# Performance work log

Hardware: AMD Instinct MI355X
Metric: run time of the kernel (lower is better)

## Reference

```python
import jax, jax.numpy as jnp
import numpy as np

N, E, B = 400000, 800000, 16384
MAX_DEG = 10  # PyG MFConv default max_degree -> 11 weight sets
EPS = 1e-5


def setup_inputs() -> dict:
    key = jax.random.key(0)
    ks = jax.random.split(key, 32)
    d = {}
    d["x"] = jax.random.normal(ks[0], (N, 8), jnp.float32)
    d["edge_index"] = jax.random.randint(ks[1], (2, E), 0, N)
    d["batch"] = jnp.sort(jax.random.randint(ks[2], (N,), 0, B))
    d["x_mord"] = jax.random.normal(ks[3], (B, 862), jnp.float32)
    D = MAX_DEG + 1
    # MFConv degree-dependent weights: Wl (with bias) applied to neighbor sum, Wr (no bias) to self.
    d["Wl1"] = jax.random.normal(ks[4], (D, 32, 8), jnp.float32) * 0.2
    d["bl1"] = jnp.zeros((D, 32), jnp.float32)
    d["Wr1"] = jax.random.normal(ks[5], (D, 32, 8), jnp.float32) * 0.2
    d["Wl2"] = jax.random.normal(ks[6], (D, 32, 32), jnp.float32) * 0.1
    d["bl2"] = jnp.zeros((D, 32), jnp.float32)
    d["Wr2"] = jax.random.normal(ks[7], (D, 32, 32), jnp.float32) * 0.1
    d["Wl3"] = jax.random.normal(ks[8], (D, 32, 32), jnp.float32) * 0.1
    d["bl3"] = jnp.zeros((D, 32), jnp.float32)
    d["Wr3"] = jax.random.normal(ks[9], (D, 32, 32), jnp.float32) * 0.1
    # Dense MLP head
    d["W_fc1"] = jax.random.normal(ks[10], (512, 862), jnp.float32) * 0.03
    d["b_fc1"] = jnp.zeros((512,), jnp.float32)
    d["g1"] = jnp.ones((512,), jnp.float32)
    d["be1"] = jnp.zeros((512,), jnp.float32)
    d["W_fc2"] = jax.random.normal(ks[11], (128, 512), jnp.float32) * 0.04
    d["b_fc2"] = jnp.zeros((128,), jnp.float32)
    d["g2"] = jnp.ones((128,), jnp.float32)
    d["be2"] = jnp.zeros((128,), jnp.float32)
    d["W_fc3"] = jax.random.normal(ks[12], (64, 128), jnp.float32) * 0.09
    d["b_fc3"] = jnp.zeros((64,), jnp.float32)
    d["g3"] = jnp.ones((64,), jnp.float32)
    d["be3"] = jnp.zeros((64,), jnp.float32)
    d["W_out"] = jax.random.normal(ks[13], (1, 96), jnp.float32) * 0.1
    d["b_out"] = jnp.zeros((1,), jnp.float32)
    return d


def _mfconv(x, src, dst, deg_idx, Wl, bl, Wr):
    # h_i = sum_{j in N(i)} x_j  (source_to_target aggregation)
    h = jax.ops.segment_sum(x[src], dst, num_segments=x.shape[0])
    Wl_n = Wl[deg_idx]   # [N, out, in]
    Wr_n = Wr[deg_idx]
    return (jnp.einsum('noi,ni->no', Wl_n, h) + bl[deg_idx]
            + jnp.einsum('noi,ni->no', Wr_n, x))


def _bn_train(h, g, b):
    mu = jnp.mean(h, axis=0)
    var = jnp.mean((h - mu) ** 2, axis=0)  # biased, as torch BN training
    return (h - mu) * jax.lax.rsqrt(var + EPS) * g + b


def reference(x, edge_index, batch, x_mord,
              Wl1, bl1, Wr1, Wl2, bl2, Wr2, Wl3, bl3, Wr3,
              W_fc1, b_fc1, g1, be1, W_fc2, b_fc2, g2, be2,
              W_fc3, b_fc3, g3, be3, W_out, b_out):
    src, dst = edge_index[0], edge_index[1]
    n = x.shape[0]
    deg = jax.ops.segment_sum(jnp.ones((src.shape[0],), jnp.float32), dst, num_segments=n)
    deg_idx = jnp.minimum(deg, MAX_DEG).astype(jnp.int32)

    h = jax.nn.relu(_mfconv(x, src, dst, deg_idx, Wl1, bl1, Wr1))
    h = jax.nn.relu(_mfconv(h, src, dst, deg_idx, Wl2, bl2, Wr2))
    h = _mfconv(h, src, dst, deg_idx, Wl3, bl3, Wr3)

    # global mean pool over graphs
    num_graphs = x_mord.shape[0]
    sums = jax.ops.segment_sum(h, batch, num_segments=num_graphs)
    cnts = jax.ops.segment_sum(jnp.ones((n,), jnp.float32), batch, num_segments=num_graphs)
    pooled = sums / jnp.maximum(cnts, 1.0)[:, None]  # [B, 32]

    m = _bn_train(jax.nn.relu(x_mord @ W_fc1.T + b_fc1), g1, be1)
    m = _bn_train(jax.nn.relu(m @ W_fc2.T + b_fc2), g2, be2)
    m = _bn_train(jax.nn.relu(m @ W_fc3.T + b_fc3), g3, be3)

    z = jnp.concatenate([pooled, m], axis=1)  # [B, 96]
    return jax.nn.sigmoid(z @ W_out.T + b_out)
```

## Files before the change

kernel.cpp:

```cpp
#include <hip/hip_runtime.h>
#include <hip/hip_bf16.h>
#include <math.h>

#define MORD 862

typedef short s16x8 __attribute__((ext_vector_type(8)));
typedef float f32x4 __attribute__((ext_vector_type(4)));

static __device__ __forceinline__ unsigned short f2bf(float v) {
  __hip_bfloat16 h = __float2bfloat16(v);
  return *(unsigned short*)&h;
}
static __device__ __forceinline__ float bf2f(unsigned short u) {
  unsigned int x = ((unsigned int)u) << 16;
  return *(float*)&x;
}

__global__ __launch_bounds__(512) void bin_scan(const int* __restrict__ bhist, int* __restrict__ boff,
                                                int* __restrict__ gcur, int nbins, int E) {
  __shared__ int ts[512];
  int tid = threadIdx.x;
  int v = (tid < nbins) ? bhist[tid] : 0;
  ts[tid] = v;
  __syncthreads();
  for (int st = 1; st < 512; st <<= 1) {
    int t = (tid >= st) ? ts[tid - st] : 0;
    __syncthreads();
    ts[tid] += t;
    __syncthreads();
  }
  int ex = ts[tid] - v;
  if (tid < nbins) { boff[tid] = ex; gcur[tid] = ex; }
  if (tid == 0) boff[nbins] = E;
}

__global__ __launch_bounds__(256) void bin_split(const int* __restrict__ srcA, const int* __restrict__ dstA,
                                                 int* __restrict__ gcur, unsigned long long* __restrict__ ebuf,
                                                 int E, int nbins) {
  __shared__ unsigned long long sbuf[512 * 8];
  __shared__ int lcur[512];
  int tid = threadIdx.x;
  for (int base = blockIdx.x * 1024; base < E; base += (int)gridDim.x * 1024) {
    for (int i = tid; i < nbins; i += 256) lcur[i] = 0;
    __syncthreads();
    int e0 = base + tid * 4;
#pragma unroll
    for (int j = 0; j < 4; j++) {
      int e = e0 + j;
      if (e < E) {
        int d = dstA[e], s = srcA[e];
        int bin = d >> 10;
        unsigned long long p = ((unsigned long long)(unsigned int)d << 32) | (unsigned int)s;
        int slot = atomicAdd(&lcur[bin], 1);
        if (slot < 8) sbuf[bin * 8 + slot] = p;
        else { int g = atomicAdd(&gcur[bin], 1); ebuf[g] = p; }
      }
    }
    __syncthreads();
    for (int b = tid; b < nbins; b += 256) {
      int cnt = min(lcur[b], 8);
      if (cnt > 0) {
        int g = atomicAdd(&gcur[b], cnt);
        for (int k = 0; k < cnt; k++) ebuf[g + k] = sbuf[b * 8 + k];
      }
    }
    __syncthreads();
  }
}

__global__ __launch_bounds__(256) void bin_csr(const unsigned long long* __restrict__ ebuf,
                                               const int* __restrict__ boff,
                                               int* __restrict__ off, int* __restrict__ csr,
                                               int N, int E) {
  __shared__ int lcur[1024];
  __shared__ int part[256];
  int b = blockIdx.x;
  int n0 = b << 10;
  int nn = min(1024, N - n0);
  int e0 = boff[b], e1 = boff[b + 1];
  int tid = threadIdx.x;
  for (int i = tid; i < nn; i += 256) lcur[i] = 0;
  __syncthreads();
  for (int e = e0 + tid; e < e1; e += 256) {
    int d = (int)(ebuf[e] >> 32);
    atomicAdd(&lcur[d - n0], 1);
  }
  __syncthreads();
  int base4 = tid * 4;
  int c0 = (base4 < nn) ? lcur[base4] : 0;
  int c1 = (base4 + 1 < nn) ? lcur[base4 + 1] : 0;
  int c2 = (base4 + 2 < nn) ? lcur[base4 + 2] : 0;
  int c3 = (base4 + 3 < nn) ? lcur[base4 + 3] : 0;
  int tot = c0 + c1 + c2 + c3;
  part[tid] = tot;
  __syncthreads();
  for (int st = 1; st < 256; st <<= 1) {
    int t = (tid >= st) ? part[tid - st] : 0;
    __syncthreads();
    part[tid] += t;
    __syncthreads();
  }
  int pre = part[tid] - tot;
  __syncthreads();
  if (base4 < nn)     { lcur[base4]     = pre;                off[n0 + base4]     = e0 + pre; }
  if (base4 + 1 < nn) { lcur[base4 + 1] = pre + c0;           off[n0 + base4 + 1] = e0 + pre + c0; }
  if (base4 + 2 < nn) { lcur[base4 + 2] = pre + c0 + c1;      off[n0 + base4 + 2] = e0 + pre + c0 + c1; }
  if (base4 + 3 < nn) { lcur[base4 + 3] = pre + c0 + c1 + c2; off[n0 + base4 + 3] = e0 + pre + c0 + c1 + c2; }
  if (b == 0 && tid == 0) off[N] = E;
  __syncthreads();
  for (int e = e0 + tid; e < e1; e += 256) {
    unsigned long long p = ebuf[e];
    int d = (int)(p >> 32);
    int s = (int)(p & 0xffffffffu);
    int slot = atomicAdd(&lcur[d - n0], 1);
    csr[e0 + slot] = s;
  }
}

__global__ __launch_bounds__(256) void mega_prep(const int* __restrict__ dstA, int* __restrict__ bhist, int E, int nbins,
                                                 const float* __restrict__ Wl1, const float* __restrict__ Wr1,
                                                 unsigned short* __restrict__ Wc1,
                                                 const float* __restrict__ Wl2, const float* __restrict__ Wr2,
                                                 unsigned short* __restrict__ Wc2,
                                                 const float* __restrict__ Wl3, const float* __restrict__ Wr3,
                                                 unsigned short* __restrict__ Wc3,
                                                 const int* __restrict__ batch, int* __restrict__ goff, int N, int B) {
  if (blockIdx.y == 0) {
    __shared__ int lh[512];
    for (int i = threadIdx.x; i < nbins; i += 256) lh[i] = 0;
    __syncthreads();
    for (int e = blockIdx.x * 256 + threadIdx.x; e < E; e += gridDim.x * 256)
      atomicAdd(&lh[dstA[e] >> 10], 1);
    __syncthreads();
    for (int i = threadIdx.x; i < nbins; i += 256)
      if (lh[i]) atomicAdd(&bhist[i], lh[i]);
    return;
  }
  int bx = blockIdx.x;
  if (bx >= 264) {
    int b = (bx - 264) * 256 + threadIdx.x;
    if (b > B) return;
    int lo = 0, hi = N;
    while (lo < hi) {
      int mid = (lo + hi) >> 1;
      if (batch[mid] < b) lo = mid + 1; else hi = mid;
    }
    goff[b] = lo;
    return;
  }
  if (bx >= 88 * 3) return;
  int set = bx / 88;
  const float* Wl = set == 0 ? Wl1 : (set == 1 ? Wl2 : Wl3);
  const float* Wr = set == 0 ? Wr1 : (set == 1 ? Wr2 : Wr3);
  unsigned short* Wc = set == 0 ? Wc1 : (set == 1 ? Wc2 : Wc3);
  int CIN = set == 0 ? 8 : 32;
  int idx = (bx - set * 88) * 256 + threadIdx.x;
  if (idx >= 352 * 64) return;
  int row = idx >> 6, k = idx & 63;
  int d = row >> 5, o = row & 31;
  float v = 0.f;
  if (k < CIN) v = Wl[((size_t)d * 32 + o) * CIN + k];
  else if (k < 2 * CIN) v = Wr[((size_t)d * 32 + o) * CIN + (k - CIN)];
  Wc[idx] = f2bf(v);
}

__global__ __launch_bounds__(256) void prep_hx1(const float* __restrict__ x, const int* __restrict__ off,
                                                const int* __restrict__ csr,
                                                unsigned short* __restrict__ x1, unsigned short* __restrict__ agg1, int N) {
  int n = blockIdx.x * 256 + threadIdx.x;
  if (n >= N) return;
  int a = off[n], b = off[n + 1];
  float ag[8] = {};
  for (int j = a; j < b; j++) {
    const float* xr = x + (size_t)csr[j] * 8;
#pragma unroll
    for (int t = 0; t < 8; t++) ag[t] += xr[t];
  }
  const float* xo = x + (size_t)n * 8;
  s16x8 w0, w1;
#pragma unroll
  for (int t = 0; t < 8; t++) {
    w0[t] = (short)f2bf(ag[t]);
    w1[t] = (short)f2bf(xo[t]);
  }
  *(s16x8*)(agg1 + (size_t)n * 8) = w0;
  *(s16x8*)(x1 + (size_t)n * 8) = w1;
}

__global__ __launch_bounds__(256) void gather_c(const unsigned short* __restrict__ X, const int* __restrict__ off,
                                                const int* __restrict__ csr, unsigned short* __restrict__ AGG, int N) {
  long long tid = (long long)blockIdx.x * 256 + threadIdx.x;
  if (tid >= (long long)N * 4) return;
  int n = (int)(tid >> 2), q = (int)(tid & 3);
  int a = off[n], b = off[n + 1];
  float s[8] = {};
  for (int j = a; j < b; j++) {
    const s16x8 v = *(const s16x8*)(X + (size_t)csr[j] * 32 + q * 8);
#pragma unroll
    for (int t = 0; t < 8; t++) s[t] += bf2f((unsigned short)v[t]);
  }
  s16x8 w;
#pragma unroll
  for (int t = 0; t < 8; t++) w[t] = (short)f2bf(s[t]);
  *(s16x8*)(AGG + (size_t)n * 32 + q * 8) = w;
}

template <int KS, int ACH, int OUTMODE>
__global__ __launch_bounds__(512, 4) void mfconv_mfma(const unsigned short* __restrict__ xin,
                                                      const unsigned short* __restrict__ agg,
                                                      const unsigned short* __restrict__ Wcat,
                                                      const float* __restrict__ bl,
                                                      const int* __restrict__ off,
                                                      unsigned short* __restrict__ outp, int N) {
  __shared__ __align__(16) unsigned short As[128 * ACH * 8];
  __shared__ __align__(16) unsigned short Bs[352 * 64];
  __shared__ float sbias[352];
  __shared__ int sdeg[128];
  const int tid = threadIdx.x;
  const int wid = tid >> 6, lane = tid & 63;

  for (int s = wid; s < 44; s += 8) {
    int c = s * 64 + lane;
    int cs = c ^ ((c >> 3) & 7);
    __builtin_amdgcn_global_load_lds((const __attribute__((address_space(1))) void*)((const char*)Wcat + (size_t)cs * 16),
                                     (__attribute__((address_space(3))) void*)((char*)Bs + s * 1024), 16, 0, 0);
  }
  for (int i = tid; i < 352; i += 512) sbias[i] = bl[i];

  const int ntiles = N >> 7;
  for (int t = blockIdx.x; t < ntiles; t += (int)gridDim.x) {
    const int row0 = t << 7;
    __syncthreads();
    for (int s = wid; s < 2 * ACH; s += 8) {
      int c = s * 64 + lane;
      int row = c / ACH, ch = c & (ACH - 1);
      int cs = ch ^ (row & (ACH - 1));
      size_t grow = (size_t)(row0 + row);
      const char* srcp;
      if (ACH == 4) {
        srcp = (cs == 1) ? (const char*)xin + grow * 16 : (const char*)agg + grow * 16;
      } else {
        srcp = (cs < 4) ? (const char*)agg + grow * 64 + (size_t)cs * 16
                        : (const char*)xin + grow * 64 + (size_t)(cs - 4) * 16;
      }
      __builtin_amdgcn_global_load_lds((const __attribute__((address_space(1))) void*)srcp,
                                       (__attribute__((address_space(3))) void*)((char*)As + s * 1024), 16, 0, 0);
    }
    if (tid < 128) sdeg[tid] = min(off[row0 + tid + 1] - off[row0 + tid], 10);
    __syncthreads();

    const int ra = wid * 16 + (lane & 15);
    const int g4 = lane >> 4;
    const int rl0 = wid * 16 + g4 * 4;
    int dj[4];
#pragma unroll
    for (int j = 0; j < 4; j++) dj[j] = sdeg[rl0 + j];

#pragma unroll
    for (int h = 0; h < 2; h++) {
      f32x4 acc[11] = {};
#pragma unroll
      for (int kk = 0; kk < KS; kk++) {
        int cha = (kk * 4 + g4) ^ (ra & (ACH - 1));
        s16x8 af = *(const s16x8*)((const char*)As + (size_t)(ra * ACH + cha) * 16);
#pragma unroll
        for (int nn = 0; nn < 11; nn++) {
          int rb = (h * 11 + nn) * 16 + (lane & 15);
          int cb = rb * 8 + kk * 4 + g4;
          s16x8 bf = *(const s16x8*)((const char*)Bs + (size_t)(cb ^ (rb & 7)) * 16);
          acc[nn] = __builtin_amdgcn_mfma_f32_16x16x32_bf16(af, bf, acc[nn], 0, 0, 0);
        }
      }
#pragma unroll
      for (int nn = 0; nn < 11; nn++) {
        int n = h * 11 + nn;
        int dsel = n >> 1;
        int o = (n & 1) * 16 + (lane & 15);
        float bv = sbias[dsel * 32 + o];
#pragma unroll
        for (int j = 0; j < 4; j++) {
          if (dj[j] == dsel) {
            float v = acc[nn][j] + bv;
            size_t gr = (size_t)row0 + rl0 + j;
            if (OUTMODE == 0) v = fmaxf(v, 0.f);
            outp[gr * 32 + o] = f2bf(v);
          }
        }
      }
    }
  }
}

__global__ __launch_bounds__(256) void cvt2(const float* __restrict__ xm, const float* __restrict__ Wf1,
                                            unsigned short* __restrict__ Abf, unsigned short* __restrict__ Bbf1, int B) {
  const int q = 224;
  int t = blockIdx.x * 256 + threadIdx.x;
  if (t >= (B + 512) * q) return;
  int r = t / q, c4 = (t % q) * 4;
  const float* srow = (r < B) ? xm + (size_t)r * MORD : Wf1 + (size_t)(r - B) * MORD;
  unsigned short* drow = (r < B) ? Abf + (size_t)r * 896 : Bbf1 + (size_t)(r - B) * 896;
#pragma unroll
  for (int j = 0; j < 4; j++) {
    int k = c4 + j;
    float v = (k < MORD) ? srow[k] : 0.f;
    drow[k] = f2bf(v);
  }
}

__global__ __launch_bounds__(256) void gemm_fc1b(const unsigned short* __restrict__ A,
                                                 const unsigned short* __restrict__ Bw,
                                                 const float* __restrict__ bias,
                                                 unsigned short* __restrict__ Cout,
                                                 float* __restrict__ csum, float* __restrict__ csq,
                                                 int M, int Nn, int Kp) {
  __shared__ __align__(16) unsigned short As[128 * 64];
  __shared__ __align__(16) unsigned short Bs[128 * 64];
  __shared__ float scs[128], sqs[128];
  int tid = threadIdx.x;
  int wid = tid >> 6, lane = tid & 63;
  int m0 = blockIdx.y * 128, n0 = blockIdx.x * 128;
  int wr = wid >> 1, wc = wid & 1;
  f32x4 acc[4][4] = {};

  int srow_l = lane >> 3;
  int scol = (lane & 7) * 8;
  int aReadBase = ((wr * 64 + (lane & 15)) * 128) + ((lane >> 4) * 16);
  int bReadBase = ((wc * 64 + (lane & 15)) * 128) + ((lane >> 4) * 16);

  const unsigned short* Ablk = A + (size_t)m0 * Kp;
  const unsigned short* Bblk = Bw + (size_t)n0 * Kp;

  for (int k0 = 0; k0 < Kp; k0 += 64) {
#pragma unroll
    for (int i = 0; i < 4; i++) {
      int s = wid * 4 + i;
      int row = s * 8 + srow_l;
      const unsigned short* ga = Ablk + (size_t)row * Kp + k0 + scol;
      const unsigned short* gb = Bblk + (size_t)row * Kp + k0 + scol;
      __builtin_amdgcn_global_load_lds((const __attribute__((address_space(1))) void*)ga,
                                       (__attribute__((address_space(3))) void*)(As + s * 512), 16, 0, 0);
      __builtin_amdgcn_global_load_lds((const __attribute__((address_space(1))) void*)gb,
                                       (__attribute__((address_space(3))) void*)(Bs + s * 512), 16, 0, 0);
    }
    __syncthreads();
#pragma unroll
    for (int kk = 0; kk < 2; kk++) {
      s16x8 af[4], bfr[4];
#pragma unroll
      for (int m = 0; m < 4; m++)
        af[m] = *(const s16x8*)((const char*)As + aReadBase + m * (16 * 128) + kk * 64);
#pragma unroll
      for (int n = 0; n < 4; n++)
        bfr[n] = *(const s16x8*)((const char*)Bs + bReadBase + n * (16 * 128) + kk * 64);
#pragma unroll
      for (int m = 0; m < 4; m++)
#pragma unroll
        for (int n = 0; n < 4; n++)
          acc[m][n] = __builtin_amdgcn_mfma_f32_16x16x32_bf16(af[m], bfr[n], acc[m][n], 0, 0, 0);
    }
    __syncthreads();
  }

  if (tid < 128) { scs[tid] = 0.f; sqs[tid] = 0.f; }
  __syncthreads();
  int rbase = m0 + wr * 64 + (lane >> 4) * 4;
  int lc = lane & 15;
#pragma unroll
  for (int n = 0; n < 4; n++) {
    int colb = wc * 64 + n * 16 + lc;
    float bv = bias[n0 + colb];
    float s = 0.f, q = 0.f;
#pragma unroll
    for (int m = 0; m < 4; m++) {
#pragma unroll
      for (int j = 0; j < 4; j++) {
        int row = rbase + m * 16 + j;
        float v = fmaxf(acc[m][n][j] + bv, 0.f);
        Cout[(size_t)row * Nn + n0 + colb] = f2bf(v);
        s += v;
        q = fmaf(v, v, q);
      }
    }
    s += __shfl_xor(s, 16); q += __shfl_xor(q, 16);
    s += __shfl_xor(s, 32); q += __shfl_xor(q, 32);
    if ((lane >> 4) == 0) { atomicAdd(&scs[colb], s); atomicAdd(&sqs[colb], q); }
  }
  __syncthreads();
  if (tid < 128) { atomicAdd(&csum[n0 + tid], scs[tid]); atomicAdd(&csq[n0 + tid], sqs[tid]); }
}

__global__ __launch_bounds__(256) void prepW2_bn(const float* __restrict__ W2, const float* __restrict__ b2,
                                                 const float* __restrict__ s1, const float* __restrict__ q1,
                                                 const float* __restrict__ g1, const float* __restrict__ be1,
                                                 unsigned short* __restrict__ W2p, float* __restrict__ b2p,
                                                 int Nn, int K, float invM) {
  __shared__ float a1l[512], h1l[512];
  for (int c = threadIdx.x; c < K; c += 256) {
    float mu = s1[c] * invM;
    float var = q1[c] * invM - mu * mu;
    float sc = g1[c] * rsqrtf(var + 1e-5f);
    a1l[c] = sc;
    h1l[c] = be1[c] - mu * sc;
  }
  __syncthreads();
  int wid = threadIdx.x >> 6, lane = threadIdx.x & 63;
  int n = blockIdx.x * 4 + wid;
  if (n >= Nn) return;
  float part = 0.f;
  for (int k = lane; k < K; k += 64) {
    float w = W2[(size_t)n * K + k];
    W2p[(size_t)n * K + k] = f2bf(w * a1l[k]);
    part = fmaf(w, h1l[k], part);
  }
#pragma unroll
  for (int off = 32; off > 0; off >>= 1) part += __shfl_down(part, off, 64);
  if (lane == 0) b2p[n] = b2[n] + part;
}

__global__ __launch_bounds__(256) void gemm_fc2(const unsigned short* __restrict__ A,
                                                const unsigned short* __restrict__ Bw,
                                                const float* __restrict__ bias,
                                                float* __restrict__ Cout,
                                                float* __restrict__ csum, float* __restrict__ csq,
                                                int M, int Nn, int Kp) {
  __shared__ __align__(16) unsigned short As[128 * 64];
  __shared__ __align__(16) unsigned short Bs[128 * 64];
  __shared__ float scs[128], sqs[128];
  int tid = threadIdx.x;
  int wid = tid >> 6, lane = tid & 63;
  int m0 = blockIdx.y * 128;
  int wr = wid >> 1, wc = wid & 1;
  f32x4 acc[4][4] = {};

  int srow_l = lane >> 3;
  int scol = (lane & 7) * 8;
  int aReadBase = ((wr * 64 + (lane & 15)) * 128) + ((lane >> 4) * 16);
  int bReadBase = ((wc * 64 + (lane & 15)) * 128) + ((lane >> 4) * 16);

  const unsigned short* Ablk = A + (size_t)m0 * Kp;

  for (int k0 = 0; k0 < Kp; k0 += 64) {
#pragma unroll
    for (int i = 0; i < 4; i++) {
      int s = wid * 4 + i;
      int row = s * 8 + srow_l;
      const unsigned short* ga = Ablk + (size_t)row * Kp + k0 + scol;
      const unsigned short* gb = Bw + (size_t)row * Kp + k0 + scol;
      __builtin_amdgcn_global_load_lds((const __attribute__((address_space(1))) void*)ga,
                                       (__attribute__((address_space(3))) void*)(As + s * 512), 16, 0, 0);
      __builtin_amdgcn_global_load_lds((const __attribute__((address_space(1))) void*)gb,
                                       (__attribute__((address_space(3))) void*)(Bs + s * 512), 16, 0, 0);
    }
    __syncthreads();
#pragma unroll
    for (int kk = 0; kk < 2; kk++) {
      s16x8 af[4], bfr[4];
#pragma unroll
      for (int m = 0; m < 4; m++)
        af[m] = *(const s16x8*)((const char*)As + aReadBase + m * (16 * 128) + kk * 64);
#pragma unroll
      for (int n = 0; n < 4; n++)
        bfr[n] = *(const s16x8*)((const char*)Bs + bReadBase + n * (16 * 128) + kk * 64);
#pragma unroll
      for (int m = 0; m < 4; m++)
#pragma unroll
        for (int n = 0; n < 4; n++)
          acc[m][n] = __builtin_amdgcn_mfma_f32_16x16x32_bf16(af[m], bfr[n], acc[m][n], 0, 0, 0);
    }
    __syncthreads();
  }

  if (tid < 128) { scs[tid] = 0.f; sqs[tid] = 0.f; }
  __syncthreads();
  int rbase = m0 + wr * 64 + (lane >> 4) * 4;
  int lc = lane & 15;
#pragma unroll
  for (int n = 0; n < 4; n++) {
    int colb = wc * 64 + n * 16 + lc;
    float bv = bias[colb];
    float s = 0.f, q = 0.f;
#pragma unroll
    for (int m = 0; m < 4; m++) {
#pragma unroll
      for (int j = 0; j < 4; j++) {
        int row = rbase + m * 16 + j;
        float v = fmaxf(acc[m][n][j] + bv, 0.f);
        Cout[(size_t)row * Nn + colb] = v;
        s += v;
        q = fmaf(v, v, q);
      }
    }
    s += __shfl_xor(s, 16); q += __shfl_xor(q, 16);
    s += __shfl_xor(s, 32); q += __shfl_xor(q, 32);
    if ((lane >> 4) == 0) { atomicAdd(&scs[colb], s); atomicAdd(&sqs[colb], q); }
  }
  __syncthreads();
  if (tid < 128) { atomicAdd(&csum[tid], scs[tid]); atomicAdd(&csq[tid], sqs[tid]); }
}

__global__ __launch_bounds__(256) void gemm_fc3(const float* __restrict__ A, const float* __restrict__ Bw,
                                                const float* __restrict__ bias,
                                                const float* __restrict__ s2v, const float* __restrict__ q2v,
                                                const float* __restrict__ g2, const float* __restrict__ be2,
                                                float* __restrict__ C, float* __restrict__ s3, float* __restrict__ q3,
                                                int M, float invM) {
  const int BM = 64, BN = 64, BK = 16, K = 128;
  __shared__ float As[BK][BM + 1];
  __shared__ float Bs[BK][BN + 1];
  __shared__ float a2l[128], h2l[128];
  __shared__ float scs[64], sqs[64];
  int tid = threadIdx.x;
  for (int c = tid; c < 128; c += 256) {
    float mu = s2v[c] * invM;
    float var = q2v[c] * invM - mu * mu;
    float sc = g2[c] * rsqrtf(var + 1e-5f);
    a2l[c] = sc;
    h2l[c] = be2[c] - mu * sc;
  }
  if (tid < 64) { scs[tid] = 0.f; sqs[tid] = 0.f; }
  __syncthreads();
  int bm = blockIdx.y * BM;
  int tr = tid / 16, tc = tid % 16;
  float acc[4][4] = {};
  for (int k0 = 0; k0 < K; k0 += BK) {
    for (int i = tid; i < BM * BK; i += 256) {
      int m = i / BK, k = i % BK;
      float v = A[(size_t)(bm + m) * K + k0 + k];
      As[k][m] = fmaf(v, a2l[k0 + k], h2l[k0 + k]);
    }
    for (int i = tid; i < BN * BK; i += 256) {
      int n = i / BK, k = i % BK;
      Bs[k][n] = Bw[(size_t)n * K + k0 + k];
    }
    __syncthreads();
#pragma unroll
    for (int k = 0; k < BK; k++) {
      float a4[4], b4[4];
#pragma unroll
      for (int xx = 0; xx < 4; xx++) a4[xx] = As[k][tr * 4 + xx];
#pragma unroll
      for (int yy = 0; yy < 4; yy++) b4[yy] = Bs[k][tc * 4 + yy];
#pragma unroll
      for (int xx = 0; xx < 4; xx++)
#pragma unroll
        for (int yy = 0; yy < 4; yy++) acc[xx][yy] = fmaf(a4[xx], b4[yy], acc[xx][yy]);
    }
    __syncthreads();
  }
#pragma unroll
  for (int yy = 0; yy < 4; yy++) {
    int n = tc * 4 + yy;
    float bv = bias[n];
    float s = 0.f, q = 0.f;
#pragma unroll
    for (int xx = 0; xx < 4; xx++) {
      int m = bm + tr * 4 + xx;
      float v = fmaxf(acc[xx][yy] + bv, 0.f);
      C[(size_t)m * 64 + n] = v;
      s += v;
      q = fmaf(v, v, q);
    }
    atomicAdd(&scs[n], s);
    atomicAdd(&sqs[n], q);
  }
  __syncthreads();
  if (tid < 64) { atomicAdd(&s3[tid], scs[tid]); atomicAdd(&q3[tid], sqs[tid]); }
}

__global__ __launch_bounds__(256) void pool_head(const unsigned short* __restrict__ H3, const int* __restrict__ goff,
                                                 const float* __restrict__ m3,
                                                 const float* __restrict__ s3, const float* __restrict__ q3,
                                                 const float* __restrict__ g3, const float* __restrict__ be3,
                                                 const float* __restrict__ Wout, const float* __restrict__ bout,
                                                 float* __restrict__ out, int B, float invM) {
  __shared__ float a3l[64], h3l[64];
  if (threadIdx.x < 64) {
    int c = threadIdx.x;
    float mu = s3[c] * invM;
    float var = q3[c] * invM - mu * mu;
    float sc = g3[c] * rsqrtf(var + 1e-5f);
    a3l[c] = sc;
    h3l[c] = be3[c] - mu * sc;
  }
  __syncthreads();
  int w = (int)((blockIdx.x * 256 + threadIdx.x) >> 6);
  if (w >= B) return;
  int lane = threadIdx.x & 63;
  int c = lane & 31, r2 = lane >> 5;
  int a = goff[w], b = goff[w + 1];
  float s = 0.f;
  for (int r = a + r2; r < b; r += 2) s += bf2f(H3[(size_t)r * 32 + c]);
  s += __shfl_down(s, 32);
  float val = 0.f;
  if (r2 == 0) val = (s / fmaxf((float)(b - a), 1.f)) * Wout[c];
  float mv = m3[(size_t)w * 64 + lane];
  val += fmaf(mv, a3l[lane], h3l[lane]) * Wout[32 + lane];
#pragma unroll
  for (int off = 32; off > 0; off >>= 1) val += __shfl_down(val, off);
  if (lane == 0) out[w] = 1.f / (1.f + expf(-(val + bout[0])));
}

extern "C" void kernel_launch(void* const* d_in, const int* in_sizes, int n_in,
                              void* d_out, int out_size, void* d_ws, size_t ws_size,
                              hipStream_t stream) {
  const float* x = (const float*)d_in[0];
  const int* eidx = (const int*)d_in[1];
  const int* batch = (const int*)d_in[2];
  const float* xmord = (const float*)d_in[3];
  const float* Wl1 = (const float*)d_in[4];
  const float* bl1 = (const float*)d_in[5];
  const float* Wr1 = (const float*)d_in[6];
  const float* Wl2 = (const float*)d_in[7];
  const float* bl2 = (const float*)d_in[8];
  const float* Wr2 = (const float*)d_in[9];
  const float* Wl3 = (const float*)d_in[10];
  const float* bl3 = (const float*)d_in[11];
  const float* Wr3 = (const float*)d_in[12];
  const float* Wf1 = (const float*)d_in[13];
  const float* bf1 = (const float*)d_in[14];
  const float* g1 = (const float*)d_in[15];
  const float* be1 = (const float*)d_in[16];
  const float* Wf2 = (const float*)d_in[17];
  const float* bf2 = (const float*)d_in[18];
  const float* g2 = (const float*)d_in[19];
  const float* be2 = (const float*)d_in[20];
  const float* Wf3 = (const float*)d_in[21];
  const float* bf3 = (const float*)d_in[22];
  const float* g3 = (const float*)d_in[23];
  const float* be3 = (const float*)d_in[24];
  const float* Wout = (const float*)d_in[25];
  const float* bout = (const float*)d_in[26];
  float* out = (float*)d_out;

  const int N = in_sizes[2];
  const int E = in_sizes[1] / 2;
  const int B = in_sizes[3] / MORD;
  const int nbins = (N + 1023) >> 10;
  const int* src = eidx;
  const int* dst = eidx + E;

  char* ws = (char*)d_ws;
  size_t off_ = 0;
  auto alloc = [&](size_t bytes) { size_t o = off_; off_ += (bytes + 255) & ~(size_t)255; return o; };
  size_t oX1 = alloc((size_t)N * 8 * 2);
  size_t oAGG1 = alloc((size_t)N * 8 * 2);
  size_t oX2 = alloc((size_t)N * 32 * 2);
  size_t oX3 = alloc((size_t)N * 32 * 2);
  size_t oAGG = alloc((size_t)N * 32 * 2);
  size_t oOff = alloc((size_t)(N + 1) * 4);
  size_t oCsr = alloc((size_t)E * 4);
  size_t oEbuf = alloc((size_t)E * 8);
  size_t oH3 = alloc((size_t)N * 32 * 2);
  size_t oGoff = alloc((size_t)(B + 1) * 4);
  size_t oStats = alloc(8192 * 4);
  size_t oWc1 = alloc(352 * 64 * 2);
  size_t oWc2 = alloc(352 * 64 * 2);
  size_t oWc3 = alloc(352 * 64 * 2);
  (void)ws_size;

  unsigned short* X1 = (unsigned short*)(ws + oX1);
  unsigned short* AGG1 = (unsigned short*)(ws + oAGG1);
  unsigned short* X2 = (unsigned short*)(ws + oX2);
  unsigned short* X3 = (unsigned short*)(ws + oX3);
  unsigned short* AGG = (unsigned short*)(ws + oAGG);
  int* offp = (int*)(ws + oOff);
  int* csr = (int*)(ws + oCsr);
  unsigned long long* ebuf = (unsigned long long*)(ws + oEbuf);
  unsigned short* H3 = (unsigned short*)(ws + oH3);
  int* goff = (int*)(ws + oGoff);
  float* st = (float*)(ws + oStats);
  int* bhist = (int*)(st + 4096);
  int* boff = (int*)(st + 4608);
  int* gcur = (int*)(st + 5184);
  unsigned short* Wc1 = (unsigned short*)(ws + oWc1);
  unsigned short* Wc2 = (unsigned short*)(ws + oWc2);
  unsigned short* Wc3 = (unsigned short*)(ws + oWc3);
  float *s1 = st, *q1 = st + 512;
  float *s2 = st + 2048, *q2 = st + 2176;
  float *s3 = st + 2560, *q3 = st + 2624;

  unsigned short* Abf = (unsigned short*)(ws + oX2);
  unsigned short* Bbf1 = (unsigned short*)(ws + oX2 + 29360128);
  unsigned short* W2p = (unsigned short*)(ws + oX2 + 29360128 + 917504);
  float* b2p = (float*)(ws + oX2 + 29360128 + 917504 + 131072);
  unsigned short* m1 = (unsigned short*)(ws + oAGG);
  float* m2 = (float*)(ws + oAGG + 16777216);
  float* m3 = (float*)(ws + oOff);

  hipMemsetAsync(st, 0, 4608 * 4, stream);

  mega_prep<<<dim3(400, 2), 256, 0, stream>>>(dst, bhist, E, nbins,
                                              Wl1, Wr1, Wc1, Wl2, Wr2, Wc2, Wl3, Wr3, Wc3,
                                              batch, goff, N, B);
  bin_scan<<<1, 512, 0, stream>>>(bhist, boff, gcur, nbins, E);
  bin_split<<<400, 256, 0, stream>>>(src, dst, gcur, ebuf, E, nbins);
  bin_csr<<<nbins, 256, 0, stream>>>(ebuf, boff, offp, csr, N, E);

  prep_hx1<<<(N + 255) / 256, 256, 0, stream>>>(x, offp, csr, X1, AGG1, N);
  mfconv_mfma<1, 4, 0><<<512, 512, 0, stream>>>(X1, AGG1, Wc1, bl1, offp, X2, N);
  gather_c<<<(int)(((long long)N * 4 + 255) / 256), 256, 0, stream>>>(X2, offp, csr, AGG, N);
  mfconv_mfma<2, 8, 0><<<512, 512, 0, stream>>>(X2, AGG, Wc2, bl2, offp, X3, N);
  gather_c<<<(int)(((long long)N * 4 + 255) / 256), 256, 0, stream>>>(X3, offp, csr, AGG, N);
  mfconv_mfma<2, 8, 1><<<512, 512, 0, stream>>>(X3, AGG, Wc3, bl3, offp, H3, N);

  cvt2<<<((B + 512) * 224 + 255) / 256, 256, 0, stream>>>(xmord, Wf1, Abf, Bbf1, B);
  gemm_fc1b<<<dim3(4, B / 128), 256, 0, stream>>>(Abf, Bbf1, bf1, m1, s1, q1, B, 512, 896);
  prepW2_bn<<<32, 256, 0, stream>>>(Wf2, bf2, s1, q1, g1, be1, W2p, b2p, 128, 512, 1.f / B);
  gemm_fc2<<<dim3(1, B / 128), 256, 0, stream>>>(m1, W2p, b2p, m2, s2, q2, B, 128, 512);
  gemm_fc3<<<dim3(1, B / 64), 256, 0, stream>>>(m2, Wf3, bf3, s2, q2, g2, be2, m3, s3, q3, B, 1.f / B);
  pool_head<<<(B * 64 + 255) / 256, 256, 0, stream>>>(H3, goff, m3, s3, q3, g3, be3, Wout, bout, out, B, 1.f / B);
}
```

Baseline: 334.3 us.

## Unroll CSR gathers by four, move Wf1 conversion into prep, swizzle fc1 tiles

The neighbor-gather loops in prep_hx1 and gather_c now handle four edges per iteration. They issue independent vector loads and mask out-of-range lanes with FMA weights, which raises memory-level parallelism on the random gathers. The Wf1 bf16 conversion moves out of cvt2 into extra blocks of mega_prep, and its buffers get dedicated workspace slots so it can run alongside the graph preprocessing. gemm_fc1b also remaps block IDs with a swizzle to improve L2 locality. The cost is a few redundant loads for the masked lanes and a larger prep grid.

```diff
diff --git a/kernel.cpp b/kernel.cpp
--- a/kernel.cpp
+++ b/kernel.cpp
@@ -6,6 +6,7 @@
 
 typedef short s16x8 __attribute__((ext_vector_type(8)));
 typedef float f32x4 __attribute__((ext_vector_type(4)));
+typedef float f32x4a __attribute__((ext_vector_type(4), aligned(4)));
 
 static __device__ __forceinline__ unsigned short f2bf(float v) {
   __hip_bfloat16 h = __float2bfloat16(v);
@@ -124,12 +125,14 @@
                                                  unsigned short* __restrict__ Wc2,
                                                  const float* __restrict__ Wl3, const float* __restrict__ Wr3,
                                                  unsigned short* __restrict__ Wc3,
-                                                 const int* __restrict__ batch, int* __restrict__ goff, int N, int B) {
+                                                 const int* __restrict__ batch, int* __restrict__ goff, int N, int B,
+                                                 const float* __restrict__ Wf1, unsigned short* __restrict__ Bbf1) {
   if (blockIdx.y == 0) {
+    if (blockIdx.x >= 400) return;
     __shared__ int lh[512];
     for (int i = threadIdx.x; i < nbins; i += 256) lh[i] = 0;
     __syncthreads();
-    for (int e = blockIdx.x * 256 + threadIdx.x; e < E; e += gridDim.x * 256)
+    for (int e = blockIdx.x * 256 + threadIdx.x; e < E; e += 400 * 256)
       atomicAdd(&lh[dstA[e] >> 10], 1);
     __syncthreads();
     for (int i = threadIdx.x; i < nbins; i += 256)
@@ -137,6 +140,18 @@
     return;
   }
   int bx = blockIdx.x;
+  if (bx >= 330) {
+    int idx = (bx - 330) * 256 + threadIdx.x;
+    if (idx >= 512 * 224) return;
+    int r = idx / 224, c4 = (idx % 224) * 4;
+#pragma unroll
+    for (int j = 0; j < 4; j++) {
+      int k = c4 + j;
+      float v = (k < MORD) ? Wf1[(size_t)r * MORD + k] : 0.f;
+      Bbf1[(size_t)r * 896 + k] = f2bf(v);
+    }
+    return;
+  }
   if (bx >= 264) {
     int b = (bx - 264) * 256 + threadIdx.x;
     if (b > B) return;
@@ -148,7 +163,6 @@
     goff[b] = lo;
     return;
   }
-  if (bx >= 88 * 3) return;
   int set = bx / 88;
   const float* Wl = set == 0 ? Wl1 : (set == 1 ? Wl2 : Wl3);
   const float* Wr = set == 0 ? Wr1 : (set == 1 ? Wr2 : Wr3);
@@ -171,10 +185,34 @@
   if (n >= N) return;
   int a = off[n], b = off[n + 1];
   float ag[8] = {};
-  for (int j = a; j < b; j++) {
-    const float* xr = x + (size_t)csr[j] * 8;
-#pragma unroll
-    for (int t = 0; t < 8; t++) ag[t] += xr[t];
+  for (int base = a; base < b; base += 4) {
+    int rem = b - base;
+    int j1 = base + (rem > 1 ? 1 : 0);
+    int j2 = base + (rem > 2 ? 2 : 0);
+    int j3 = base + (rem > 3 ? 3 : 0);
+    int cc0 = csr[base], cc1 = csr[j1], cc2 = csr[j2], cc3 = csr[j3];
+    f32x4a v0a = *(const f32x4a*)(x + (size_t)cc0 * 8);
+    f32x4a v0b = *(const f32x4a*)(x + (size_t)cc0 * 8 + 4);
+    f32x4a v1a = *(const f32x4a*)(x + (size_t)cc1 * 8);
+    f32x4a v1b = *(const f32x4a*)(x + (size_t)cc1 * 8 + 4);
+    f32x4a v2a = *(const f32x4a*)(x + (size_t)cc2 * 8);
+    f32x4a v2b = *(const f32x4a*)(x + (size_t)cc2 * 8 + 4);
+    f32x4a v3a = *(const f32x4a*)(x + (size_t)cc3 * 8);
+    f32x4a v3b = *(const f32x4a*)(x + (size_t)cc3 * 8 + 4);
+    float m1 = rem > 1 ? 1.f : 0.f;
+    float m2 = rem > 2 ? 1.f : 0.f;
+    float m3 = rem > 3 ? 1.f : 0.f;
+#pragma unroll
+    for (int t = 0; t < 4; t++) {
+      ag[t] += v0a[t];
+      ag[t] = fmaf(m1, v1a[t], ag[t]);
+      ag[t] = fmaf(m2, v2a[t], ag[t]);
+      ag[t] = fmaf(m3, v3a[t], ag[t]);
+      ag[t + 4] += v0b[t];
+      ag[t + 4] = fmaf(m1, v1b[t], ag[t + 4]);
+      ag[t + 4] = fmaf(m2, v2b[t], ag[t + 4]);
+      ag[t + 4] = fmaf(m3, v3b[t], ag[t + 4]);
+    }
   }
   const float* xo = x + (size_t)n * 8;
   s16x8 w0, w1;
@@ -194,10 +232,26 @@
   int n = (int)(tid >> 2), q = (int)(tid & 3);
   int a = off[n], b = off[n + 1];
   float s[8] = {};
-  for (int j = a; j < b; j++) {
-    const s16x8 v = *(const s16x8*)(X + (size_t)csr[j] * 32 + q * 8);
-#pragma unroll
-    for (int t = 0; t < 8; t++) s[t] += bf2f((unsigned short)v[t]);
+  for (int base = a; base < b; base += 4) {
+    int rem = b - base;
+    int j1 = base + (rem > 1 ? 1 : 0);
+    int j2 = base + (rem > 2 ? 2 : 0);
+    int j3 = base + (rem > 3 ? 3 : 0);
+    int cc0 = csr[base], cc1 = csr[j1], cc2 = csr[j2], cc3 = csr[j3];
+    const s16x8 v0 = *(const s16x8*)(X + (size_t)cc0 * 32 + q * 8);
+    const s16x8 v1 = *(const s16x8*)(X + (size_t)cc1 * 32 + q * 8);
+    const s16x8 v2 = *(const s16x8*)(X + (size_t)cc2 * 32 + q * 8);
+    const s16x8 v3 = *(const s16x8*)(X + (size_t)cc3 * 32 + q * 8);
+    float m1 = rem > 1 ? 1.f : 0.f;
+    float m2 = rem > 2 ? 1.f : 0.f;
+    float m3 = rem > 3 ? 1.f : 0.f;
+#pragma unroll
+    for (int t = 0; t < 8; t++) {
+      s[t] += bf2f((unsigned short)v0[t]);
+      s[t] = fmaf(m1, bf2f((unsigned short)v1[t]), s[t]);
+      s[t] = fmaf(m2, bf2f((unsigned short)v2[t]), s[t]);
+      s[t] = fmaf(m3, bf2f((unsigned short)v3[t]), s[t]);
+    }
   }
   s16x8 w;
 #pragma unroll
@@ -291,19 +345,16 @@
   }
 }
 
-__global__ __launch_bounds__(256) void cvt2(const float* __restrict__ xm, const float* __restrict__ Wf1,
-                                            unsigned short* __restrict__ Abf, unsigned short* __restrict__ Bbf1, int B) {
+__global__ __launch_bounds__(256) void cvtA(const float* __restrict__ xm, unsigned short* __restrict__ Abf, int B) {
   const int q = 224;
   int t = blockIdx.x * 256 + threadIdx.x;
-  if (t >= (B + 512) * q) return;
+  if (t >= B * q) return;
   int r = t / q, c4 = (t % q) * 4;
-  const float* srow = (r < B) ? xm + (size_t)r * MORD : Wf1 + (size_t)(r - B) * MORD;
-  unsigned short* drow = (r < B) ? Abf + (size_t)r * 896 : Bbf1 + (size_t)(r - B) * 896;
 #pragma unroll
   for (int j = 0; j < 4; j++) {
     int k = c4 + j;
-    float v = (k < MORD) ? srow[k] : 0.f;
-    drow[k] = f2bf(v);
+    float v = (k < MORD) ? xm[(size_t)r * MORD + k] : 0.f;
+    Abf[(size_t)r * 896 + k] = f2bf(v);
   }
 }
 
@@ -318,7 +369,9 @@
   __shared__ float scs[128], sqs[128];
   int tid = threadIdx.x;
   int wid = tid >> 6, lane = tid & 63;
-  int m0 = blockIdx.y * 128, n0 = blockIdx.x * 128;
+  int lin = blockIdx.x + blockIdx.y * 4;
+  int swz = (lin & 7) * 64 + (lin >> 3);
+  int m0 = (swz >> 2) * 128, n0 = (swz & 3) * 128;
   int wr = wid >> 1, wc = wid & 1;
   f32x4 acc[4][4] = {};
 
@@ -656,6 +709,8 @@
   size_t oWc1 = alloc(352 * 64 * 2);
   size_t oWc2 = alloc(352 * 64 * 2);
   size_t oWc3 = alloc(352 * 64 * 2);
+  size_t oBbf1 = alloc(512 * 896 * 2);
+  size_t oW2p = alloc(128 * 512 * 2 + 1024);
   (void)ws_size;
 
   unsigned short* X1 = (unsigned short*)(ws + oX1);
@@ -675,23 +730,23 @@
   unsigned short* Wc1 = (unsigned short*)(ws + oWc1);
   unsigned short* Wc2 = (unsigned short*)(ws + oWc2);
   unsigned short* Wc3 = (unsigned short*)(ws + oWc3);
+  unsigned short* Bbf1 = (unsigned short*)(ws + oBbf1);
+  unsigned short* W2p = (unsigned short*)(ws + oW2p);
+  float* b2p = (float*)(ws + oW2p + 131072);
   float *s1 = st, *q1 = st + 512;
   float *s2 = st + 2048, *q2 = st + 2176;
   float *s3 = st + 2560, *q3 = st + 2624;
 
   unsigned short* Abf = (unsigned short*)(ws + oX2);
-  unsigned short* Bbf1 = (unsigned short*)(ws + oX2 + 29360128);
-  unsigned short* W2p = (unsigned short*)(ws + oX2 + 29360128 + 917504);
-  float* b2p = (float*)(ws + oX2 + 29360128 + 917504 + 131072);
   unsigned short* m1 = (unsigned short*)(ws + oAGG);
   float* m2 = (float*)(ws + oAGG + 16777216);
   float* m3 = (float*)(ws + oOff);
 
   hipMemsetAsync(st, 0, 4608 * 4, stream);
 
-  mega_prep<<<dim3(400, 2), 256, 0, stream>>>(dst, bhist, E, nbins,
+  mega_prep<<<dim3(778, 2), 256, 0, stream>>>(dst, bhist, E, nbins,
                                               Wl1, Wr1, Wc1, Wl2, Wr2, Wc2, Wl3, Wr3, Wc3,
-                                              batch, goff, N, B);
+                                              batch, goff, N, B, Wf1, Bbf1);
   bin_scan<<<1, 512, 0, stream>>>(bhist, boff, gcur, nbins, E);
   bin_split<<<400, 256, 0, stream>>>(src, dst, gcur, ebuf, E, nbins);
   bin_csr<<<nbins, 256, 0, stream>>>(ebuf, boff, offp, csr, N, E);
@@ -703,7 +758,7 @@
   gather_c<<<(int)(((long long)N * 4 + 255) / 256), 256, 0, stream>>>(X3, offp, csr, AGG, N);
   mfconv_mfma<2, 8, 1><<<512, 512, 0, stream>>>(X3, AGG, Wc3, bl3, offp, H3, N);
 
-  cvt2<<<((B + 512) * 224 + 255) / 256, 256, 0, stream>>>(xmord, Wf1, Abf, Bbf1, B);
+  cvtA<<<(B * 224 + 255) / 256, 256, 0, stream>>>(xmord, Abf, B);
   gemm_fc1b<<<dim3(4, B / 128), 256, 0, stream>>>(Abf, Bbf1, bf1, m1, s1, q1, B, 512, 896);
   prepW2_bn<<<32, 256, 0, stream>>>(Wf2, bf2, s1, q1, g1, be1, W2p, b2p, 128, 512, 1.f / B);
   gemm_fc2<<<dim3(1, B / 128), 256, 0, stream>>>(m1, W2p, b2p, m2, s2, q2, B, 128, 512);
```

After: 327.0 us. 2.2% less time.
